# Kernel optimization log

Hardware: AMD Instinct MI355X
Metric: run time of the kernel (lower is better)

## Reference

```python
import jax, jax.numpy as jnp
import numpy as np

IN_DIM = 256
OUT_DIM = 256

def setup_inputs() -> dict:
    key = jax.random.key(0)
    k1, k2, k3, k4 = jax.random.split(key, 4)
    B, N, K, D = 4, 10000, 16, IN_DIM
    x = jax.random.normal(k1, (B, N, D), dtype=jnp.float32)
    neigh = jax.random.randint(k2, (N, K), 0, N, dtype=jnp.int64)
    # nn.Linear(2*in_dim, out_dim): W [out, 2*in], b [out]
    bound = 1.0 / np.sqrt(2 * D)
    W = jax.random.uniform(k3, (OUT_DIM, 2 * D), minval=-bound, maxval=bound, dtype=jnp.float32)
    b = jax.random.uniform(k4, (OUT_DIM,), minval=-bound, maxval=bound, dtype=jnp.float32)
    return {"x": x, "neigh": neigh, "W": W, "b": b}

def reference(x, neigh, W, b):
    # x: [B,N,D], neigh: [N,K] with -1 = padding
    mask = (neigh >= 0)                                # [N,K]
    idx = jnp.clip(neigh, 0, None)                     # [N,K]
    # batch_gather_nodes: x_nei[b,n,k,:] = x[b, idx[n,k], :]
    x_nei = x[:, idx, :]                               # [B,N,K,D]
    x_nei = x_nei * mask[None, :, :, None].astype(x.dtype)
    denom = jnp.clip(mask.sum(axis=1), 1, None).astype(x.dtype)  # [N]
    agg = x_nei.sum(axis=2) / denom[None, :, None]     # [B,N,D]
    h = jnp.concatenate([x, agg], axis=-1)             # [B,N,2D]
    return jax.nn.relu(jnp.einsum('bnd,od->bno', h, W) + b)
```

## Files before the change

kernel.cpp:

```cpp
#include <hip/hip_runtime.h>
#include <hip/hip_bf16.h>
#include <stdint.h>

#define B_   4
#define N_   10000
#define K_   16
#define D_   256
#define OUT_ 256
#define M_   (B_ * N_)
#define TILES_ 625
#define TPH    16384

#define C16_ELEMS ((size_t)M_ * 16)
#define C8_ELEMS  ((size_t)M_ * 8)

typedef __attribute__((ext_vector_type(8))) short          short8;
typedef __attribute__((ext_vector_type(8))) unsigned short ushort8;
typedef __attribute__((ext_vector_type(4))) float          f32x4;
typedef __attribute__((ext_vector_type(4))) unsigned short ushort4_t;

__device__ inline unsigned short f2bf(float f) {
    __hip_bfloat16 h = __float2bfloat16(f);
    return *reinterpret_cast<unsigned short*>(&h);
}
__device__ inline float bf2f(unsigned short u) {
    unsigned int v = ((unsigned int)u) << 16;
    return __builtin_bit_cast(float, v);
}

__global__ __launch_bounds__(256) void wprep(const float* __restrict__ W,
                                             unsigned short* __restrict__ Wb) {
    const int g  = blockIdx.x * 256 + threadIdx.x;
    const int h  = g >> 14;
    const int t  = g & 16383;
    const int ks = t >> 12;
    const int rr = (t >> 4) & 255;
    const int kg = (t & 15) * 4;
    const float4 v = *(const float4*)(W + (size_t)rr * 512 + h * 256 + ks * 64 + kg);
    ushort4_t s;
    s.x = f2bf(v.x); s.y = f2bf(v.y); s.z = f2bf(v.z); s.w = f2bf(v.w);
    const int off = ((rr * 128 + kg * 2) ^ ((rr & 7) << 4)) >> 1;
    *(ushort4_t*)(Wb + (size_t)(h * 4 + ks) * TPH + off) = s;
}

__global__ __launch_bounds__(512) void gemm3(const float* __restrict__ x,
                                             const unsigned short* __restrict__ Wb,
                                             float* __restrict__ y1c,
                                             unsigned short* __restrict__ y2c) {
    __shared__ unsigned short As[64 * 64];
    __shared__ unsigned short Bs[256 * 64];

    const int tid  = threadIdx.x;
    const int w    = tid >> 6;
    const int lane = tid & 63;
    const int q    = lane >> 4;
    const int r16  = lane & 15;
    const int wm   = w >> 2;
    const int wn   = w & 3;

    const int bi   = blockIdx.x;
    const int xcd  = bi & 7;
    const int u    = bi >> 3;
    const int g    = (u >> 1) * 8 + xcd;
    const int half = u & 1;
    if (g >= TILES_) return;
    const int tile_m = g * 64;

    const int arow = tid >> 3;
    const int akg  = (tid & 7) * 8;
    const float* ap = x + (size_t)(tile_m + arow) * D_ + akg;
    const unsigned int awoff = (unsigned)((arow * 128 + akg * 2) ^ ((arow & 7) << 4));

    const unsigned short* wsrc0 = Wb + (size_t)(half * 4) * TPH + tid * 8;

    const unsigned int sw = (unsigned)((r16 & 7) << 4);

    f32x4 acc[2][4] = {};

    float4 c0 = *(const float4*)ap;
    float4 c1 = *(const float4*)(ap + 4);
#pragma unroll
    for (int i2 = 0; i2 < 4; ++i2) {
        __builtin_amdgcn_global_load_lds(
            (const __attribute__((address_space(1))) void*)(wsrc0 + i2 * 4096),
            (__attribute__((address_space(3))) void*)(Bs + tid * 8 + i2 * 4096),
            16, 0, 0);
    }
    {
        ushort8 s;
        s[0] = f2bf(c0.x); s[1] = f2bf(c0.y); s[2] = f2bf(c0.z); s[3] = f2bf(c0.w);
        s[4] = f2bf(c1.x); s[5] = f2bf(c1.y); s[6] = f2bf(c1.z); s[7] = f2bf(c1.w);
        *(ushort8*)((char*)As + awoff) = s;
    }
    __syncthreads();

#pragma unroll
    for (int ks = 0; ks < 4; ++ks) {
        float4 n0, n1;
        if (ks < 3) {
            n0 = *(const float4*)(ap + (ks + 1) * 64);
            n1 = *(const float4*)(ap + (ks + 1) * 64 + 4);
        }

#pragma unroll
        for (int ksub = 0; ksub < 2; ++ksub) {
            short8 a[2], bf[4];
#pragma unroll
            for (int i = 0; i < 2; ++i) {
                const unsigned int ad =
                    (unsigned)((wm * 32 + i * 16 + r16) * 128 + ksub * 64 + q * 16) ^ sw;
                a[i] = *(const short8*)((const char*)As + ad);
            }
#pragma unroll
            for (int j = 0; j < 4; ++j) {
                const unsigned int bd =
                    (unsigned)((wn * 64 + j * 16 + r16) * 128 + ksub * 64 + q * 16) ^ sw;
                bf[j] = *(const short8*)((const char*)Bs + bd);
            }
#pragma unroll
            for (int i = 0; i < 2; ++i)
#pragma unroll
                for (int j = 0; j < 4; ++j)
                    acc[i][j] = __builtin_amdgcn_mfma_f32_16x16x32_bf16(bf[j], a[i], acc[i][j], 0, 0, 0);
        }

        if (ks < 3) {
            __syncthreads();
            const unsigned short* wsrc = wsrc0 + (size_t)(ks + 1) * TPH;
#pragma unroll
            for (int i2 = 0; i2 < 4; ++i2) {
                __builtin_amdgcn_global_load_lds(
                    (const __attribute__((address_space(1))) void*)(wsrc + i2 * 4096),
                    (__attribute__((address_space(3))) void*)(Bs + tid * 8 + i2 * 4096),
                    16, 0, 0);
            }
            ushort8 s;
            s[0] = f2bf(n0.x); s[1] = f2bf(n0.y); s[2] = f2bf(n0.z); s[3] = f2bf(n0.w);
            s[4] = f2bf(n1.x); s[5] = f2bf(n1.y); s[6] = f2bf(n1.z); s[7] = f2bf(n1.w);
            *(ushort8*)((char*)As + awoff) = s;
            __syncthreads();
        }
    }

#pragma unroll
    for (int i = 0; i < 2; ++i) {
        const int m  = tile_m + wm * 32 + i * 16 + r16;
        const int bb = (m >= N_) + (m >= 2 * N_) + (m >= 3 * N_);
        const int n  = m - bb * N_;
        const size_t row = (size_t)(n * B_ + bb);
        if (half == 0) {
#pragma unroll
            for (int j = 0; j < 4; ++j) {
                const int o2 = wn * 64 + j * 16 + q * 4;
                f32x4 p;
                p[0] = acc[i][j][0]; p[1] = acc[i][j][1];
                p[2] = acc[i][j][2]; p[3] = acc[i][j][3];
                *(f32x4*)(y1c + (size_t)(o2 >> 3) * C8_ELEMS + row * 8 + (o2 & 7)) = p;
            }
        } else {
#pragma unroll
            for (int j = 0; j < 4; ++j) {
                const int o2 = wn * 64 + j * 16 + q * 4;
                ushort4_t p;
                p.x = f2bf(acc[i][j][0]); p.y = f2bf(acc[i][j][1]);
                p.z = f2bf(acc[i][j][2]); p.w = f2bf(acc[i][j][3]);
                *(ushort4_t*)(y2c + (size_t)(o2 >> 4) * C16_ELEMS + row * 16 + (o2 & 15)) = p;
            }
        }
    }
}

__global__ __launch_bounds__(128) void gather_out(const unsigned short* __restrict__ y2c,
                                                  const float* __restrict__ y1c,
                                                  const int*   __restrict__ neigh,
                                                  const float* __restrict__ bias,
                                                  float* __restrict__ out) {
    const int bi  = blockIdx.x;
    const int lo  = bi < 5000;
    const int c   = (bi & 7) + (lo ? 0 : 8);
    const int g   = (lo ? bi : bi - 5000) >> 3;
    const int n0  = g * 16;
    const int tid = threadIdx.x;

    __shared__ int   idx_s[16 * K_];
    __shared__ float inv_s[16];

    idx_s[tid]       = neigh[n0 * K_ + tid];
    idx_s[tid + 128] = neigh[n0 * K_ + tid + 128];
    __syncthreads();
    if (tid < 16) {
        int cnt = 0;
#pragma unroll
        for (int k = 0; k < K_; ++k) cnt += idx_s[tid * K_ + k] >= 0 ? 1 : 0;
        inv_s[tid] = 1.0f / (float)(cnt > 1 ? cnt : 1);
    }
    __syncthreads();

    const int h  = tid & 1;
    const int tl = tid >> 1;
    const int ns = tl >> 2;
    const int b  = tl & 3;

    const unsigned short* ycc = y2c + (size_t)c * C16_ELEMS;

    int jj[K_];
#pragma unroll
    for (int k = 0; k < K_; ++k) jj[k] = idx_s[ns * K_ + k];

    ushort8 vv[K_];
#pragma unroll
    for (int k = 0; k < K_; ++k) {
        const int jc = jj[k] >= 0 ? jj[k] : 0;
        vv[k] = *(const ushort8*)(ycc + ((size_t)jc * B_ + b) * 16 + h * 8);
    }

    const size_t row = (size_t)((n0 + ns) * B_ + b);
    const float* yrow = y1c + (size_t)(2 * c + h) * C8_ELEMS + row * 8;
    const f32x4 s0 = *(const f32x4*)(yrow);
    const f32x4 s1 = *(const f32x4*)(yrow + 4);
    const f32x4 b0 = *(const f32x4*)(bias + c * 16 + h * 8);
    const f32x4 b1 = *(const f32x4*)(bias + c * 16 + h * 8 + 4);

    float acc[8] = {0.f, 0.f, 0.f, 0.f, 0.f, 0.f, 0.f, 0.f};
#pragma unroll
    for (int k = 0; k < K_; ++k) {
        const float m = jj[k] >= 0 ? 1.f : 0.f;
#pragma unroll
        for (int e = 0; e < 8; ++e) acc[e] += bf2f(vv[k][e]) * m;
    }
    const float inv = inv_s[ns];

    f32x4 o0, o1;
#pragma unroll
    for (int e = 0; e < 4; ++e) {
        float v0 = acc[e] * inv + s0[e] + b0[e];
        float v1 = acc[e + 4] * inv + s1[e] + b1[e];
        o0[e] = v0 > 0.f ? v0 : 0.f;
        o1[e] = v1 > 0.f ? v1 : 0.f;
    }
    float* op = out + ((size_t)b * N_ + n0 + ns) * OUT_ + c * 16 + h * 8;
    __builtin_nontemporal_store(o0, (f32x4*)op);
    __builtin_nontemporal_store(o1, (f32x4*)(op + 4));
}

extern "C" void kernel_launch(void* const* d_in, const int* in_sizes, int n_in,
                              void* d_out, int out_size, void* d_ws, size_t ws_size,
                              hipStream_t stream) {
    const float* x     = (const float*)d_in[0];
    const int*   neigh = (const int*)d_in[1];
    const float* W     = (const float*)d_in[2];
    const float* bias  = (const float*)d_in[3];
    float*       out   = (float*)d_out;

    unsigned short* Wb  = (unsigned short*)d_ws;
    float*          y1c = (float*)(Wb + 8 * TPH);
    unsigned short* y2c = (unsigned short*)(y1c + 32 * C8_ELEMS);
    
    wprep<<<128, 256, 0, stream>>>(W, Wb);
    gemm3<<<158 * 8, 512, 0, stream>>>(x, Wb, y1c, y2c);
    gather_out<<<10000, 128, 0, stream>>>(y2c, y1c, neigh, bias, out);
}
```

Measured before the change: 157.2 us.

## Hold weight fragments in registers and run persistent GEMM without LDS

The GEMM kernel is rewritten so that each wave loads its share of the bf16 weight matrix once, pre-arranged in MFMA fragment order, and keeps it in registers (32 short8 per lane). Blocks then loop persistently over 16-row tiles of x, converting x straight into A fragments with no shared-memory staging and no barriers. This removes the per-tile re-streaming of weights through LDS and the synchronisation cost. The trade-offs are high register pressure, which may lower occupancy, and smaller 16-row M tiles with less latency hiding on the x loads.

```diff
diff --git a/kernel.cpp b/kernel.cpp
--- a/kernel.cpp
+++ b/kernel.cpp
@@ -8,8 +8,6 @@
 #define D_   256
 #define OUT_ 256
 #define M_   (B_ * N_)
-#define TILES_ 625
-#define TPH    16384
 
 #define C16_ELEMS ((size_t)M_ * 16)
 #define C8_ELEMS  ((size_t)M_ * 8)
@@ -29,141 +27,91 @@
 }
 
 __global__ __launch_bounds__(256) void wprep(const float* __restrict__ W,
-                                             unsigned short* __restrict__ Wb) {
-    const int g  = blockIdx.x * 256 + threadIdx.x;
-    const int h  = g >> 14;
-    const int t  = g & 16383;
-    const int ks = t >> 12;
-    const int rr = (t >> 4) & 255;
-    const int kg = (t & 15) * 4;
-    const float4 v = *(const float4*)(W + (size_t)rr * 512 + h * 256 + ks * 64 + kg);
+                                             unsigned short* __restrict__ WbF) {
+    const int u  = blockIdx.x * 256 + threadIdx.x;
+    const int e0 = (u & 1) * 4;
+    const int l  = (u >> 1) & 63;
+    const int v  = u >> 7;
+    const int kf = v & 7;
+    const int o16 = v >> 3;
+    const int op  = o16 * 16 + (l & 15);
+    const int k   = kf * 32 + (l >> 4) * 8 + e0;
+    const int row = (op < OUT_) ? op : op - OUT_;
+    const int col = (op < OUT_) ? k : 256 + k;
+    const float4 w4 = *(const float4*)(W + (size_t)row * 512 + col);
     ushort4_t s;
-    s.x = f2bf(v.x); s.y = f2bf(v.y); s.z = f2bf(v.z); s.w = f2bf(v.w);
-    const int off = ((rr * 128 + kg * 2) ^ ((rr & 7) << 4)) >> 1;
-    *(ushort4_t*)(Wb + (size_t)(h * 4 + ks) * TPH + off) = s;
-}
-
-__global__ __launch_bounds__(512) void gemm3(const float* __restrict__ x,
-                                             const unsigned short* __restrict__ Wb,
-                                             float* __restrict__ y1c,
-                                             unsigned short* __restrict__ y2c) {
-    __shared__ unsigned short As[64 * 64];
-    __shared__ unsigned short Bs[256 * 64];
-
+    s.x = f2bf(w4.x); s.y = f2bf(w4.y); s.z = f2bf(w4.z); s.w = f2bf(w4.w);
+    *(ushort4_t*)(WbF + (size_t)u * 4) = s;
+}
+
+__global__ __launch_bounds__(256) void gemm_regB(const float* __restrict__ x,
+                                                 const unsigned short* __restrict__ WbF,
+                                                 float* __restrict__ y1c,
+                                                 unsigned short* __restrict__ y2c) {
     const int tid  = threadIdx.x;
-    const int w    = tid >> 6;
+    const int wid  = tid >> 6;
     const int lane = tid & 63;
     const int q    = lane >> 4;
     const int r16  = lane & 15;
-    const int wm   = w >> 2;
-    const int wn   = w & 3;
 
     const int bi   = blockIdx.x;
     const int xcd  = bi & 7;
-    const int u    = bi >> 3;
-    const int g    = (u >> 1) * 8 + xcd;
-    const int half = u & 1;
-    if (g >= TILES_) return;
-    const int tile_m = g * 64;
-
-    const int arow = tid >> 3;
-    const int akg  = (tid & 7) * 8;
-    const float* ap = x + (size_t)(tile_m + arow) * D_ + akg;
-    const unsigned int awoff = (unsigned)((arow * 128 + akg * 2) ^ ((arow & 7) << 4));
-
-    const unsigned short* wsrc0 = Wb + (size_t)(half * 4) * TPH + tid * 8;
-
-    const unsigned int sw = (unsigned)((r16 & 7) << 4);
-
-    f32x4 acc[2][4] = {};
-
-    float4 c0 = *(const float4*)ap;
-    float4 c1 = *(const float4*)(ap + 4);
-#pragma unroll
-    for (int i2 = 0; i2 < 4; ++i2) {
-        __builtin_amdgcn_global_load_lds(
-            (const __attribute__((address_space(1))) void*)(wsrc0 + i2 * 4096),
-            (__attribute__((address_space(3))) void*)(Bs + tid * 8 + i2 * 4096),
-            16, 0, 0);
-    }
-    {
-        ushort8 s;
-        s[0] = f2bf(c0.x); s[1] = f2bf(c0.y); s[2] = f2bf(c0.z); s[3] = f2bf(c0.w);
-        s[4] = f2bf(c1.x); s[5] = f2bf(c1.y); s[6] = f2bf(c1.z); s[7] = f2bf(c1.w);
-        *(ushort8*)((char*)As + awoff) = s;
-    }
-    __syncthreads();
-
-#pragma unroll
-    for (int ks = 0; ks < 4; ++ks) {
-        float4 n0, n1;
-        if (ks < 3) {
-            n0 = *(const float4*)(ap + (ks + 1) * 64);
-            n1 = *(const float4*)(ap + (ks + 1) * 64 + 4);
+    const int half = (bi >> 3) & 1;
+    const int slot = bi >> 4;
+
+    short8 Bfr[4][8];
+    const int o16b = half * 16 + wid * 4;
+#pragma unroll
+    for (int j = 0; j < 4; ++j)
+#pragma unroll
+        for (int kf = 0; kf < 8; ++kf)
+            Bfr[j][kf] = *(const short8*)(
+                WbF + (((size_t)(o16b + j) * 8 + kf) * 64 + lane) * 8);
+
+    for (int g = xcd + 8 * slot; g < 2500; g += 256) {
+        const int m0 = g * 16;
+        const float* xr = x + (size_t)(m0 + r16) * D_ + q * 8;
+
+        float4 xb[16];
+#pragma unroll
+        for (int kf = 0; kf < 8; ++kf) {
+            xb[2 * kf]     = *(const float4*)(xr + kf * 32);
+            xb[2 * kf + 1] = *(const float4*)(xr + kf * 32 + 4);
         }
 
-#pragma unroll
-        for (int ksub = 0; ksub < 2; ++ksub) {
-            short8 a[2], bf[4];
-#pragma unroll
-            for (int i = 0; i < 2; ++i) {
-                const unsigned int ad =
-                    (unsigned)((wm * 32 + i * 16 + r16) * 128 + ksub * 64 + q * 16) ^ sw;
-                a[i] = *(const short8*)((const char*)As + ad);
-            }
-#pragma unroll
-            for (int j = 0; j < 4; ++j) {
-                const unsigned int bd =
-                    (unsigned)((wn * 64 + j * 16 + r16) * 128 + ksub * 64 + q * 16) ^ sw;
-                bf[j] = *(const short8*)((const char*)Bs + bd);
-            }
-#pragma unroll
-            for (int i = 0; i < 2; ++i)
-#pragma unroll
-                for (int j = 0; j < 4; ++j)
-                    acc[i][j] = __builtin_amdgcn_mfma_f32_16x16x32_bf16(bf[j], a[i], acc[i][j], 0, 0, 0);
+        f32x4 acc[4] = {};
+#pragma unroll
+        for (int kf = 0; kf < 8; ++kf) {
+            short8 a;
+            a[0] = (short)f2bf(xb[2 * kf].x);     a[1] = (short)f2bf(xb[2 * kf].y);
+            a[2] = (short)f2bf(xb[2 * kf].z);     a[3] = (short)f2bf(xb[2 * kf].w);
+            a[4] = (short)f2bf(xb[2 * kf + 1].x); a[5] = (short)f2bf(xb[2 * kf + 1].y);
+            a[6] = (short)f2bf(xb[2 * kf + 1].z); a[7] = (short)f2bf(xb[2 * kf + 1].w);
+#pragma unroll
+            for (int j = 0; j < 4; ++j)
+                acc[j] = __builtin_amdgcn_mfma_f32_16x16x32_bf16(Bfr[j][kf], a, acc[j], 0, 0, 0);
         }
 
-        if (ks < 3) {
-            __syncthreads();
-            const unsigned short* wsrc = wsrc0 + (size_t)(ks + 1) * TPH;
-#pragma unroll
-            for (int i2 = 0; i2 < 4; ++i2) {
-                __builtin_amdgcn_global_load_lds(
-                    (const __attribute__((address_space(1))) void*)(wsrc + i2 * 4096),
-                    (__attribute__((address_space(3))) void*)(Bs + tid * 8 + i2 * 4096),
-                    16, 0, 0);
-            }
-            ushort8 s;
-            s[0] = f2bf(n0.x); s[1] = f2bf(n0.y); s[2] = f2bf(n0.z); s[3] = f2bf(n0.w);
-            s[4] = f2bf(n1.x); s[5] = f2bf(n1.y); s[6] = f2bf(n1.z); s[7] = f2bf(n1.w);
-            *(ushort8*)((char*)As + awoff) = s;
-            __syncthreads();
-        }
-    }
-
-#pragma unroll
-    for (int i = 0; i < 2; ++i) {
-        const int m  = tile_m + wm * 32 + i * 16 + r16;
+        const int m  = m0 + r16;
         const int bb = (m >= N_) + (m >= 2 * N_) + (m >= 3 * N_);
         const int n  = m - bb * N_;
         const size_t row = (size_t)(n * B_ + bb);
         if (half == 0) {
 #pragma unroll
             for (int j = 0; j < 4; ++j) {
-                const int o2 = wn * 64 + j * 16 + q * 4;
+                const int o2 = wid * 64 + j * 16 + q * 4;
                 f32x4 p;
-                p[0] = acc[i][j][0]; p[1] = acc[i][j][1];
-                p[2] = acc[i][j][2]; p[3] = acc[i][j][3];
+                p[0] = acc[j][0]; p[1] = acc[j][1];
+                p[2] = acc[j][2]; p[3] = acc[j][3];
                 *(f32x4*)(y1c + (size_t)(o2 >> 3) * C8_ELEMS + row * 8 + (o2 & 7)) = p;
             }
         } else {
 #pragma unroll
             for (int j = 0; j < 4; ++j) {
-                const int o2 = wn * 64 + j * 16 + q * 4;
+                const int o2 = wid * 64 + j * 16 + q * 4;
                 ushort4_t p;
-                p.x = f2bf(acc[i][j][0]); p.y = f2bf(acc[i][j][1]);
-                p.z = f2bf(acc[i][j][2]); p.w = f2bf(acc[i][j][3]);
+                p.x = f2bf(acc[j][0]); p.y = f2bf(acc[j][1]);
+                p.z = f2bf(acc[j][2]); p.w = f2bf(acc[j][3]);
                 *(ushort4_t*)(y2c + (size_t)(o2 >> 4) * C16_ELEMS + row * 16 + (o2 & 15)) = p;
             }
         }
@@ -252,11 +200,11 @@
     const float* bias  = (const float*)d_in[3];
     float*       out   = (float*)d_out;
 
-    unsigned short* Wb  = (unsigned short*)d_ws;
-    float*          y1c = (float*)(Wb + 8 * TPH);
+    unsigned short* WbF = (unsigned short*)d_ws;
+    float*          y1c = (float*)(WbF + 131072);
     unsigned short* y2c = (unsigned short*)(y1c + 32 * C8_ELEMS);
-    
-    wprep<<<128, 256, 0, stream>>>(W, Wb);
-    gemm3<<<158 * 8, 512, 0, stream>>>(x, Wb, y1c, y2c);
+
+    wprep<<<128, 256, 0, stream>>>(W, WbF);
+    gemm_regB<<<512, 256, 0, stream>>>(x, WbF, y1c, y2c);
     gather_out<<<10000, 128, 0, stream>>>(y2c, y1c, neigh, bias, out);
 }
```

Measured after the change: 201.0 us. 27.9% more time.
